# Optimization experiments

Measured on AMD Instinct MI355X. Metric: run time of the kernel, lower is better.

The kernel has to match this reference:

```python
import jax, jax.numpy as jnp
import numpy as np

ENT = 16
INNER = 64
NEG = 1e12

def _rope_sin_cos(seq_len, dim, dtype):
    # interleaved sinusoidal: pos_emb[s] = [sin0, cos0, sin1, cos1, ...]
    pos = jnp.arange(seq_len, dtype=jnp.float32)[:, None]          # [S,1]
    freqs = jnp.power(10000.0, -2.0 * jnp.arange(dim // 2, dtype=jnp.float32) / dim)
    ang = pos * freqs                                              # [S,D/2]
    sin = jnp.repeat(jnp.sin(ang), 2, axis=-1).astype(dtype)       # [S,D] (each value doubled)
    cos = jnp.repeat(jnp.cos(ang), 2, axis=-1).astype(dtype)       # [S,D]
    return sin[None, :, None, :], cos[None, :, None, :]            # broadcast to [B,S,E,D]

def _rotate_half_interleaved(x):
    # stack([-x[...,1::2], x[...,0::2]], -1).reshape(x.shape)
    return jnp.stack([-x[..., 1::2], x[..., 0::2]], axis=-1).reshape(x.shape)

def setup_inputs() -> dict:
    key = jax.random.key(0)
    k1, k2 = jax.random.split(key)
    B, S, H = 4, 1024, 1024
    last_hidden_state = jax.random.normal(k1, (B, S, H), dtype=jnp.float32)
    W_dense = jax.random.normal(k2, (H, ENT * INNER * 2), dtype=jnp.float32) * (1.0 / np.sqrt(H))
    b_dense = jnp.zeros((ENT * INNER * 2,), dtype=jnp.float32)
    token_lengh = jnp.ones((B, S), dtype=jnp.float32)  # 0/1 padding mask over key positions
    return {"last_hidden_state": last_hidden_state, "W_dense": W_dense,
            "b_dense": b_dense, "token_lengh": token_lengh}

def reference(last_hidden_state, W_dense, b_dense, token_lengh):
    B, S, H = last_hidden_state.shape
    # dense -> [B,S,E,2D]; split into q,k heads per entity type
    out = (last_hidden_state @ W_dense + b_dense).reshape(B, S, ENT, 2 * INNER)
    qw, kw = out[..., :INNER], out[..., INNER:]
    # inline RoPE
    sin, cos = _rope_sin_cos(S, INNER, qw.dtype)
    qw = qw * cos + _rotate_half_interleaved(qw) * sin
    kw = kw * cos + _rotate_half_interleaved(kw) * sin
    # pairwise biaffine scores per entity type
    logits = jnp.einsum('bmhd,bnhd->bhmn', qw, kw)                 # [B,E,S,S]
    # padding mask (key dim only, matching the torch expand semantics)
    pad = token_lengh[:, None, None, :]                            # [B,1,1,S]
    logits = logits * pad - (1.0 - pad) * NEG
    # strict lower-triangular mask (spans with end < start are invalid)
    tril = jnp.tril(jnp.ones((S, S), dtype=logits.dtype), -1)
    logits = logits - tril * NEG
    return logits / jnp.sqrt(jnp.asarray(INNER, dtype=logits.dtype))
```

## Files before the change

### kernel.cpp

```cpp
#include <hip/hip_runtime.h>
#include <hip/hip_bf16.h>
#include <stdint.h>

#define B_   4
#define S_   1024
#define H_   1024
#define NH_  16
#define D_   64
#define N1_  2048
#define M1_  4096
#define NEG_ 1000000000000.0f

typedef __attribute__((ext_vector_type(8))) short bf16x8;
typedef __attribute__((ext_vector_type(4))) float f32x4;

__device__ inline void gload_lds16(const void* g, void* l) {
  __builtin_amdgcn_global_load_lds(
      (const __attribute__((address_space(1))) unsigned int*)g,
      (__attribute__((address_space(3))) unsigned int*)l, 16, 0, 0);
}

__device__ inline unsigned short f2bf(float f) {
  union { float f; uint32_t u; } a; a.f = f;
  uint32_t r = a.u + 0x7fff + ((a.u >> 16) & 1);
  return (unsigned short)(r >> 16);
}


__global__ __launch_bounds__(256) void k_prep(
    const float4* __restrict__ lhs4, unsigned short* __restrict__ lhsb,
    const float* __restrict__ W, unsigned short* __restrict__ WT,
    float* __restrict__ tab) {
  __shared__ float tsm[32][33];
  int b = blockIdx.x, t = threadIdx.x;
  if (b < 4096) {
    int i = b * 256 + t;
    float4 v = lhs4[i];
    uint64_t pk = (uint64_t)f2bf(v.x) | ((uint64_t)f2bf(v.y) << 16) |
                  ((uint64_t)f2bf(v.z) << 32) | ((uint64_t)f2bf(v.w) << 48);
    ((uint64_t*)lhsb)[i] = pk;
  } else if (b < 6144) {
    int bb = b - 4096;
    int nb = (bb & 63) * 32, kb = (bb >> 6) * 32;
    int tx = t & 31, ty = t >> 5;
    for (int r = 0; r < 4; r++)
      tsm[ty + r * 8][tx] = W[(size_t)(kb + ty + r * 8) * N1_ + nb + tx];
    __syncthreads();
    for (int r = 0; r < 4; r++)
      WT[(size_t)(nb + ty + r * 8) * H_ + kb + tx] = f2bf(tsm[tx][ty + r * 8]);
  } else {
    int i = (b - 6144) * 256 + t;
    int pos = i >> 5, fi = i & 31;
    float freq = exp2f(-(float)fi * (13.2877123795494f / 32.0f));
    float ang = (float)pos * freq;
    tab[2 * i]     = sinf(ang);
    tab[2 * i + 1] = cosf(ang);
  }
}


__global__ __launch_bounds__(256) void k_gemm1(
    const unsigned short* __restrict__ A,
    const unsigned short* __restrict__ BT,
    const float* __restrict__ bias,
    const float* __restrict__ sc,
    unsigned short* __restrict__ qws,
    unsigned short* __restrict__ kws) {
  __shared__ unsigned short a_lds[128 * 32];
  __shared__ unsigned short b_lds[128 * 32];
  int t = threadIdx.x;
  int lane = t & 63, wv = t >> 6;
  int wm = wv >> 1, wn = wv & 1;
  int col = lane & 15, quad = lane >> 4;

  int l = blockIdx.x;
  int xcd = l & 7, k = l >> 3;
  int mBase = (((k & 3) << 3) + xcd) * 128;
  int nBase = (k >> 2) * 128;

  f32x4 acc[4][4] = {};

  for (int kk = 0; kk < H_; kk += 32) {
    for (int c = 0; c < 2; c++) {
      int idx = c * 256 + t;
      int r = idx >> 2, ch = idx & 3;
      gload_lds16(A + (size_t)(mBase + r) * H_ + kk + ch * 8, a_lds + idx * 8);
      gload_lds16(BT + (size_t)(nBase + r) * H_ + kk + ch * 8, b_lds + idx * 8);
    }
    __syncthreads();
    bf16x8 af[4], bf[4];
#pragma unroll
    for (int i = 0; i < 4; i++)
      af[i] = *(const bf16x8*)&a_lds[(wm * 64 + i * 16 + col) * 32 + quad * 8];
#pragma unroll
    for (int j = 0; j < 4; j++)
      bf[j] = *(const bf16x8*)&b_lds[(wn * 64 + j * 16 + col) * 32 + quad * 8];
#pragma unroll
    for (int j = 0; j < 4; j++)
#pragma unroll
      for (int i = 0; i < 4; i++)
        acc[j][i] = __builtin_amdgcn_mfma_f32_16x16x32_bf16(bf[j], af[i], acc[j][i], 0, 0, 0);
    __syncthreads();
  }

#pragma unroll
  for (int i = 0; i < 4; i++) {
    int m = mBase + wm * 64 + i * 16 + col;
    int pos = m & (S_ - 1);
    int bb = m >> 10;
#pragma unroll
    for (int j = 0; j < 4; j++) {
      int n = nBase + wn * 64 + j * 16 + quad * 4;
      int d = n & 63;
      int head = n >> 7;
      int isK = (n >> 6) & 1;
      float4 bj  = *(const float4*)&bias[n];
      float4 scv = *(const float4*)&sc[(pos * 32 + (d >> 1)) * 2];
      float v0 = acc[j][i][0] + bj.x;
      float v1 = acc[j][i][1] + bj.y;
      float v2 = acc[j][i][2] + bj.z;
      float v3 = acc[j][i][3] + bj.w;
      float o0 = v0 * scv.y - v1 * scv.x;
      float o1 = v1 * scv.y + v0 * scv.x;
      float o2 = v2 * scv.w - v3 * scv.z;
      float o3 = v3 * scv.w + v2 * scv.z;
      unsigned short* dst = isK ? kws : qws;
      ushort4 pk;
      pk.x = f2bf(o0); pk.y = f2bf(o1); pk.z = f2bf(o2); pk.w = f2bf(o3);
      *(ushort4*)&dst[((size_t)(bb * NH_ + head) * S_ + pos) * D_ + d] = pk;
    }
  }
}


#define STG_ 132

__global__ __launch_bounds__(256) void k_gemm2(
    const unsigned short* __restrict__ qws,
    const unsigned short* __restrict__ kws,
    const float* __restrict__ tl,
    float* __restrict__ out) {
  __shared__ __align__(16) char smem[64 * STG_ * 4];
  unsigned short* q_lds = (unsigned short*)smem;
  unsigned short* k_lds = q_lds + 128 * 64;
  float* stage = (float*)smem;

  int t = threadIdx.x;
  int lane = t & 63, wv = t >> 6, wm = wv >> 1, wn = wv & 1;
  int col = lane & 15, quad = lane >> 4;

  int l = blockIdx.x;
  int xcd = l & 7, k = l >> 3;
  int z = (xcd << 3) + (k >> 6);
  int tile = k & 63;
  int mT = (tile >> 3) * 128, nT = (tile & 7) * 128;

  const unsigned short* qb = qws + ((size_t)z * S_ + mT) * D_;
  const unsigned short* kb = kws + ((size_t)z * S_ + nT) * D_;

  for (int c = 0; c < 4; c++) {
    int idx = c * 256 + t;
    gload_lds16(qb + idx * 8, q_lds + idx * 8);
    gload_lds16(kb + idx * 8, k_lds + idx * 8);
  }
  __syncthreads();

  f32x4 acc[4][4] = {};
#pragma unroll
  for (int kk = 0; kk < 64; kk += 32) {
    bf16x8 qf[4], kf[4];
#pragma unroll
    for (int i = 0; i < 4; i++)
      qf[i] = *(const bf16x8*)&q_lds[(wm * 64 + i * 16 + col) * 64 + kk + quad * 8];
#pragma unroll
    for (int j = 0; j < 4; j++)
      kf[j] = *(const bf16x8*)&k_lds[(wn * 64 + j * 16 + col) * 64 + kk + quad * 8];
#pragma unroll
    for (int j = 0; j < 4; j++)
#pragma unroll
      for (int i = 0; i < 4; i++)
        acc[j][i] = __builtin_amdgcn_mfma_f32_16x16x32_bf16(kf[j], qf[i], acc[j][i], 0, 0, 0);
  }
  __syncthreads();

  int bb = z >> 4;
#pragma unroll
  for (int half = 0; half < 2; half++) {
    if (wm == half) {
#pragma unroll
      for (int i = 0; i < 4; i++) {
        int rloc = i * 16 + col;
#pragma unroll
        for (int j = 0; j < 4; j++) {
          int cloc = wn * 64 + j * 16 + quad * 4;
          float4 v;
          v.x = acc[j][i][0]; v.y = acc[j][i][1];
          v.z = acc[j][i][2]; v.w = acc[j][i][3];
          *(float4*)&stage[rloc * STG_ + cloc] = v;
        }
      }
    }
    __syncthreads();
    int mbase = mT + half * 64;
#pragma unroll
    for (int r = 0; r < 8; r++) {
      int f = r * 256 + t;
      int rloc = f >> 5;
      int c4 = (f & 31) * 4;
      float4 v = *(const float4*)&stage[rloc * STG_ + c4];
      int m = mbase + rloc;
      int n = nT + c4;
      float4 pad4 = *(const float4*)&tl[bb * S_ + n];
      f32x4 o;
      float x;
      x = v.x * pad4.x - (1.0f - pad4.x) * NEG_; if (m > n)     x -= NEG_; o.x = x * 0.125f;
      x = v.y * pad4.y - (1.0f - pad4.y) * NEG_; if (m > n + 1) x -= NEG_; o.y = x * 0.125f;
      x = v.z * pad4.z - (1.0f - pad4.z) * NEG_; if (m > n + 2) x -= NEG_; o.z = x * 0.125f;
      x = v.w * pad4.w - (1.0f - pad4.w) * NEG_; if (m > n + 3) x -= NEG_; o.w = x * 0.125f;
      __builtin_nontemporal_store(o, (f32x4*)&out[((size_t)z * S_ + m) * S_ + n]);
    }
    __syncthreads();
  }
}


extern "C" void kernel_launch(void* const* d_in, const int* in_sizes, int n_in,
                              void* d_out, int out_size, void* d_ws, size_t ws_size,
                              hipStream_t stream) {
  const float* lhs  = (const float*)d_in[0];
  const float* W    = (const float*)d_in[1];
  const float* bias = (const float*)d_in[2];
  const float* tl   = (const float*)d_in[3];
  float* out = (float*)d_out;

  char* ws = (char*)d_ws;
  unsigned short* lhsb = (unsigned short*)(ws);
  unsigned short* WT   = (unsigned short*)(ws + (8u  << 20));
  unsigned short* qws  = (unsigned short*)(ws + (12u << 20));
  unsigned short* kws  = (unsigned short*)(ws + (20u << 20));
  float*          sc   = (float*)        (ws + (28u << 20));

  k_prep<<<6272, 256, 0, stream>>>((const float4*)lhs, lhsb, W, WT, sc);
  k_gemm1<<<512, 256, 0, stream>>>(lhsb, WT, bias, sc, qws, kws);
  k_gemm2<<<4096, 256, 0, stream>>>(qws, kws, tl, out);
}
```

Baseline: 315.8 us.

## Skip matmul for fully masked lower tiles and loop over key tiles per block

The score kernel now launches one block per (batch-head, query tile) and loops over key tiles instead of launching one block per output tile. Tiles lying entirely below the diagonal skip the K load and the MFMA work and just store the masked constant, treating the finite logit as negligible next to the large negative offset. Remaining tiles double-buffer the K tile loads in LDS and keep the Q fragments in registers across iterations. This cuts matmul and load work, but gives 8x fewer blocks and uneven per-block work, which may hurt occupancy and store bandwidth.

```diff
diff --git a/kernel.cpp b/kernel.cpp
--- a/kernel.cpp
+++ b/kernel.cpp
@@ -140,86 +140,124 @@
     const unsigned short* __restrict__ kws,
     const float* __restrict__ tl,
     float* __restrict__ out) {
-  __shared__ __align__(16) char smem[64 * STG_ * 4];
-  unsigned short* q_lds = (unsigned short*)smem;
-  unsigned short* k_lds = q_lds + 128 * 64;
-  float* stage = (float*)smem;
+  __shared__ __align__(16) char smem[32 * 1024 + 64 * STG_ * 4];
+  unsigned short* k_lds = (unsigned short*)smem;
+  float* stage = (float*)(smem + 32 * 1024);
+  unsigned short* q_lds = (unsigned short*)(smem + 32 * 1024);
 
   int t = threadIdx.x;
   int lane = t & 63, wv = t >> 6, wm = wv >> 1, wn = wv & 1;
   int col = lane & 15, quad = lane >> 4;
 
   int l = blockIdx.x;
-  int xcd = l & 7, k = l >> 3;
-  int z = (xcd << 3) + (k >> 6);
-  int tile = k & 63;
-  int mT = (tile >> 3) * 128, nT = (tile & 7) * 128;
+  int xcd = l & 7;
+  int z = (xcd << 3) + (l >> 6);
+  int mtile = (l >> 3) & 7;
+  int mT = mtile * 128;
+  int bb = z >> 4;
 
   const unsigned short* qb = qws + ((size_t)z * S_ + mT) * D_;
-  const unsigned short* kb = kws + ((size_t)z * S_ + nT) * D_;
+  const unsigned short* kbase = kws + (size_t)z * S_ * D_;
 
   for (int c = 0; c < 4; c++) {
     int idx = c * 256 + t;
     gload_lds16(qb + idx * 8, q_lds + idx * 8);
-    gload_lds16(kb + idx * 8, k_lds + idx * 8);
-  }
-  __syncthreads();
-
-  f32x4 acc[4][4] = {};
-#pragma unroll
-  for (int kk = 0; kk < 64; kk += 32) {
-    bf16x8 qf[4], kf[4];
-#pragma unroll
-    for (int i = 0; i < 4; i++)
-      qf[i] = *(const bf16x8*)&q_lds[(wm * 64 + i * 16 + col) * 64 + kk + quad * 8];
-#pragma unroll
-    for (int j = 0; j < 4; j++)
-      kf[j] = *(const bf16x8*)&k_lds[(wn * 64 + j * 16 + col) * 64 + kk + quad * 8];
-#pragma unroll
-    for (int j = 0; j < 4; j++)
-#pragma unroll
-      for (int i = 0; i < 4; i++)
-        acc[j][i] = __builtin_amdgcn_mfma_f32_16x16x32_bf16(kf[j], qf[i], acc[j][i], 0, 0, 0);
-  }
-  __syncthreads();
-
-  int bb = z >> 4;
-#pragma unroll
-  for (int half = 0; half < 2; half++) {
-    if (wm == half) {
-#pragma unroll
-      for (int i = 0; i < 4; i++) {
-        int rloc = i * 16 + col;
-#pragma unroll
-        for (int j = 0; j < 4; j++) {
-          int cloc = wn * 64 + j * 16 + quad * 4;
-          float4 v;
-          v.x = acc[j][i][0]; v.y = acc[j][i][1];
-          v.z = acc[j][i][2]; v.w = acc[j][i][3];
-          *(float4*)&stage[rloc * STG_ + cloc] = v;
-        }
-      }
-    }
-    __syncthreads();
-    int mbase = mT + half * 64;
-#pragma unroll
-    for (int r = 0; r < 8; r++) {
-      int f = r * 256 + t;
-      int rloc = f >> 5;
-      int c4 = (f & 31) * 4;
-      float4 v = *(const float4*)&stage[rloc * STG_ + c4];
-      int m = mbase + rloc;
-      int n = nT + c4;
+    gload_lds16(kbase + (size_t)mT * D_ + idx * 8, k_lds + idx * 8);
+  }
+
+  {
+    int c4 = (t & 31) * 4;
+    int r0 = t >> 5;
+    for (int nt = 0; nt < mtile; nt++) {
+      int n = nt * 128 + c4;
       float4 pad4 = *(const float4*)&tl[bb * S_ + n];
       f32x4 o;
       float x;
-      x = v.x * pad4.x - (1.0f - pad4.x) * NEG_; if (m > n)     x -= NEG_; o.x = x * 0.125f;
-      x = v.y * pad4.y - (1.0f - pad4.y) * NEG_; if (m > n + 1) x -= NEG_; o.y = x * 0.125f;
-      x = v.z * pad4.z - (1.0f - pad4.z) * NEG_; if (m > n + 2) x -= NEG_; o.z = x * 0.125f;
-      x = v.w * pad4.w - (1.0f - pad4.w) * NEG_; if (m > n + 3) x -= NEG_; o.w = x * 0.125f;
-      __builtin_nontemporal_store(o, (f32x4*)&out[((size_t)z * S_ + m) * S_ + n]);
-    }
-    __syncthreads();
+      x = 0.0f * pad4.x - (1.0f - pad4.x) * NEG_; x -= NEG_; o.x = x * 0.125f;
+      x = 0.0f * pad4.y - (1.0f - pad4.y) * NEG_; x -= NEG_; o.y = x * 0.125f;
+      x = 0.0f * pad4.z - (1.0f - pad4.z) * NEG_; x -= NEG_; o.z = x * 0.125f;
+      x = 0.0f * pad4.w - (1.0f - pad4.w) * NEG_; x -= NEG_; o.w = x * 0.125f;
+#pragma unroll
+      for (int r = 0; r < 16; r++) {
+        int m = mT + r * 8 + r0;
+        __builtin_nontemporal_store(o, (f32x4*)&out[((size_t)z * S_ + m) * S_ + n]);
+      }
+    }
+  }
+
+  __syncthreads();
+
+  bf16x8 qf[2][4];
+#pragma unroll
+  for (int kk2 = 0; kk2 < 2; kk2++)
+#pragma unroll
+    for (int i = 0; i < 4; i++)
+      qf[kk2][i] = *(const bf16x8*)&q_lds[(wm * 64 + i * 16 + col) * 64 + kk2 * 32 + quad * 8];
+  __syncthreads();
+
+  int cur = 0;
+  for (int nt = mtile; nt < 8; nt++) {
+    int nT = nt * 128;
+    if (nt + 1 < 8) {
+      const unsigned short* kb = kbase + (size_t)(nT + 128) * D_;
+      for (int c = 0; c < 4; c++) {
+        int idx = c * 256 + t;
+        gload_lds16(kb + idx * 8, k_lds + (cur ^ 1) * 8192 + idx * 8);
+      }
+    }
+    bf16x8 kf[2][4];
+#pragma unroll
+    for (int kk2 = 0; kk2 < 2; kk2++)
+#pragma unroll
+      for (int j = 0; j < 4; j++)
+        kf[kk2][j] = *(const bf16x8*)&k_lds[cur * 8192 + (wn * 64 + j * 16 + col) * 64 + kk2 * 32 + quad * 8];
+    f32x4 acc[4][4] = {};
+#pragma unroll
+    for (int kk2 = 0; kk2 < 2; kk2++)
+#pragma unroll
+      for (int j = 0; j < 4; j++)
+#pragma unroll
+        for (int i = 0; i < 4; i++)
+          acc[j][i] = __builtin_amdgcn_mfma_f32_16x16x32_bf16(kf[kk2][j], qf[kk2][i], acc[j][i], 0, 0, 0);
+
+#pragma unroll
+    for (int half = 0; half < 2; half++) {
+      if (wm == half) {
+#pragma unroll
+        for (int i = 0; i < 4; i++) {
+          int rloc = i * 16 + col;
+#pragma unroll
+          for (int j = 0; j < 4; j++) {
+            int cloc = wn * 64 + j * 16 + quad * 4;
+            float4 v;
+            v.x = acc[j][i][0]; v.y = acc[j][i][1];
+            v.z = acc[j][i][2]; v.w = acc[j][i][3];
+            *(float4*)&stage[rloc * STG_ + cloc] = v;
+          }
+        }
+      }
+      __syncthreads();
+      int mbase = mT + half * 64;
+#pragma unroll
+      for (int r = 0; r < 8; r++) {
+        int f = r * 256 + t;
+        int rloc = f >> 5;
+        int c4 = (f & 31) * 4;
+        float4 v = *(const float4*)&stage[rloc * STG_ + c4];
+        int m = mbase + rloc;
+        int n = nT + c4;
+        float4 pad4 = *(const float4*)&tl[bb * S_ + n];
+        f32x4 o;
+        float x;
+        x = v.x * pad4.x - (1.0f - pad4.x) * NEG_; if (m > n)     x -= NEG_; o.x = x * 0.125f;
+        x = v.y * pad4.y - (1.0f - pad4.y) * NEG_; if (m > n + 1) x -= NEG_; o.y = x * 0.125f;
+        x = v.z * pad4.z - (1.0f - pad4.z) * NEG_; if (m > n + 2) x -= NEG_; o.z = x * 0.125f;
+        x = v.w * pad4.w - (1.0f - pad4.w) * NEG_; if (m > n + 3) x -= NEG_; o.w = x * 0.125f;
+        __builtin_nontemporal_store(o, (f32x4*)&out[((size_t)z * S_ + m) * S_ + n]);
+      }
+      __syncthreads();
+    }
+    cur ^= 1;
   }
 }
 
@@ -242,5 +280,5 @@
 
   k_prep<<<6272, 256, 0, stream>>>((const float4*)lhs, lhsb, W, WT, sc);
   k_gemm1<<<512, 256, 0, stream>>>(lhsb, WT, bias, sc, qws, kws);
-  k_gemm2<<<4096, 256, 0, stream>>>(qws, kws, tl, out);
-}
+  k_gemm2<<<512, 256, 0, stream>>>(qws, kws, tl, out);
+}
```

New measurement: 330.6 us. 4.7% more time.
